# Optimization experiments

Measured on AMD Instinct MI355X. Metric: run time of the kernel, lower is better.

The kernel has to match this reference:

```python
import jax, jax.numpy as jnp
import numpy as np

K = 8  # knn_graph(k=8, loop=True): self-loop kept, so self is among the k nearest


def knn_idx(x, k):
    # x: [N, F]. Pairwise squared distances via the expansion trick.
    x2 = jnp.sum(x * x, axis=-1)                      # [N]
    d = x2[:, None] + x2[None, :] - 2.0 * (x @ x.T)   # [N, N]
    _, idx = jax.lax.top_k(-d, k)                     # [N, k] nearest (incl. self)
    return idx


def edge_conv(x, idx, W1, b1, W2, b2):
    # PyG EdgeConv: message = nn(cat([x_i, x_j - x_i])), aggr='max'.
    # Every node has exactly k incoming edges, so scatter-max == max over the k axis.
    n, f = x.shape
    k = idx.shape[1]
    xi = x[:, None, :]                                # [N, 1, F] center
    xj = x[idx]                                       # [N, k, F] neighbors (gather)
    e = jnp.concatenate([jnp.broadcast_to(xi, (n, k, f)), xj - xi], axis=-1)  # [N,k,2F]
    h = jax.nn.relu(e @ W1 + b1) @ W2 + b2            # [N, k, out]
    return jnp.max(h, axis=1)                         # [N, out]


def setup_inputs() -> dict:
    key = jax.random.key(0)
    ks = jax.random.split(key, 9)
    B, N, F = 2, 4096, 3
    H0, H1, OUT = 64, 128, 256

    def lin(kw, fan_in, fan_out):
        bound = 1.0 / np.sqrt(fan_in)
        kw1, kw2 = jax.random.split(kw)
        W = jax.random.uniform(kw1, (fan_in, fan_out), jnp.float32, -bound, bound)
        b = jax.random.uniform(kw2, (fan_out,), jnp.float32, -bound, bound)
        return W, b

    W1, b1 = lin(ks[0], 2 * F, H0)
    W2, b2 = lin(ks[1], H0, H1)
    W3, b3 = lin(ks[2], 2 * H1, H1)
    W4, b4 = lin(ks[3], H1, OUT)
    point_cloud = jax.random.normal(ks[4], (B, N, F), jnp.float32)
    return {"point_cloud": point_cloud, "W1": W1, "b1": b1, "W2": W2, "b2": b2,
            "W3": W3, "b3": b3, "W4": W4, "b4": b4}


def reference(point_cloud, W1, b1, W2, b2, W3, b3, W4, b4):
    B, N, F = point_cloud.shape
    pts = point_cloud.reshape(B * N, F)               # knn over ALL B*N points (no batch vec)
    idx = knn_idx(jax.lax.stop_gradient(pts), K)      # [B*N, K]
    x = jax.nn.relu(edge_conv(pts, idx, W1, b1, W2, b2))
    x = edge_conv(x, idx, W3, b3, W4, b4)
    return x.reshape(B, N, -1)
```

## Files before the change

### kernel.cpp

```cpp
#include <hip/hip_runtime.h>

#define NPTS 8192
#define NSLICE 64
#define SLICE_LEN (NPTS / NSLICE)
#define KNN 8
#define SURV_CAP 32
#define TQ 32

typedef short bf16x8 __attribute__((ext_vector_type(8)));
typedef float f32x4 __attribute__((ext_vector_type(4)));

__device__ __forceinline__ unsigned short f2bf(float x) {
  unsigned int u = __float_as_uint(x);
  return (unsigned short)((u + 0x7FFF + ((u >> 16) & 1)) >> 16);
}
__device__ __forceinline__ float bf2f(unsigned short s) {
  return __uint_as_float(((unsigned int)s) << 16);
}

__device__ __forceinline__ float dist_exact(float qx, float qy, float qz,
                                            float q2, float px, float py,
                                            float pz, float p2) {
#pragma clang fp contract(off)
  float dot = __fmaf_rn(qz, pz, __fmaf_rn(qy, py, __fmul_rn(qx, px)));
  float t1 = __fadd_rn(q2, p2);
  return __fadd_rn(t1, __fmul_rn(-2.0f, dot));
}

__device__ __forceinline__ float norm2_exact(float x, float y, float z) {
#pragma clang fp contract(off)
  return __fadd_rn(__fadd_rn(__fmul_rn(x, x), __fmul_rn(y, y)),
                   __fmul_rn(z, z));
}

__device__ __forceinline__ float med3(float a, float b, float c) {
  return __builtin_amdgcn_fmed3f(a, b, c);
}

__device__ __forceinline__ double pack_key(float d, int idx) {
  unsigned int ub = __float_as_uint(d);
  ub ^= (((unsigned int)((int)ub >> 31)) | 0x80000000u);
  unsigned int lo = (ub << 13) | (unsigned int)idx;
  unsigned int hi = 0x3ff00000u | (ub >> 19);
  return __hiloint2double((int)hi, (int)lo);
}

#define KEY_DECL                                                            \
  const double KINF = __longlong_as_double(0x7ff0000000000000LL);           \
  double k0 = KINF, k1 = KINF, k2 = KINF, k3 = KINF, k4 = KINF, k5 = KINF,  \
         k6 = KINF, k7 = KINF;
#define KB1(s)                                                              \
  {                                                                         \
    double mn = fmin(carry, k##s);                                          \
    carry = fmax(carry, k##s);                                              \
    k##s = mn;                                                              \
  }
#define KEY_INSERT(key)                                                     \
  {                                                                         \
    double carry = (key);                                                   \
    KB1(0) KB1(1) KB1(2) KB1(3) KB1(4) KB1(5) KB1(6) KB1(7)                 \
  }

#define VINS(dv)                                                            \
  {                                                                         \
    float dd = (dv);                                                        \
    v7 = med3(dd, v6, v7);                                                  \
    v6 = med3(dd, v5, v6);                                                  \
    v5 = med3(dd, v4, v5);                                                  \
    v4 = med3(dd, v3, v4);                                                  \
    v3 = med3(dd, v2, v3);                                                  \
    v2 = med3(dd, v1, v2);                                                  \
    v1 = med3(dd, v0, v1);                                                  \
    v0 = fminf(dd, v0);                                                     \
  }

#define VDECL                                                               \
  const float FINF = __uint_as_float(0x7f800000u);                          \
  float v0 = FINF, v1 = FINF, v2 = FINF, v3 = FINF, v4 = FINF, v5 = FINF,   \
        v6 = FINF, v7 = FINF;

__global__ __launch_bounds__(256) void prep_kernel(
    const float* __restrict__ W4, const float* __restrict__ pts,
    unsigned short* __restrict__ W4ht, unsigned short* __restrict__ W4lt,
    float4* __restrict__ pts4) {
  const int id = blockIdx.x * 256 + threadIdx.x;
  const int k = id >> 8, c = id & 255;
  float v = W4[k * 256 + c];
  unsigned short hi = f2bf(v);
  unsigned short lo = f2bf(v - bf2f(hi));
  W4ht[c * 128 + k] = hi;
  W4lt[c * 128 + k] = lo;
  if (id < NPTS) {
    float x = pts[id * 3 + 0];
    float y = pts[id * 3 + 1];
    float z = pts[id * 3 + 2];
    pts4[id] = make_float4(x, y, z, norm2_exact(x, y, z));
  }
}

__global__ __launch_bounds__(256) void knn_vals_kernel(
    const float4* __restrict__ pts4, float* __restrict__ part_v) {
  __shared__ float4 sp[SLICE_LEN];
  const int t = threadIdx.x;
  const int q = blockIdx.x * 256 + t;
  const int jbase = blockIdx.y * SLICE_LEN;
  for (int p = t; p < SLICE_LEN; p += 256) sp[p] = pts4[jbase + p];
  __syncthreads();
  const float4 qp = pts4[q];
  const float qx = qp.x, qy = qp.y, qz = qp.z, q2 = qp.w;
  VDECL;
  for (int p = 0; p < SLICE_LEN; p += 8) {
    float4 c0 = sp[p + 0];
    float4 c1 = sp[p + 1];
    float4 c2 = sp[p + 2];
    float4 c3 = sp[p + 3];
    float4 c4 = sp[p + 4];
    float4 c5 = sp[p + 5];
    float4 c6 = sp[p + 6];
    float4 c7 = sp[p + 7];
    float d0 = dist_exact(qx, qy, qz, q2, c0.x, c0.y, c0.z, c0.w);
    float d1 = dist_exact(qx, qy, qz, q2, c1.x, c1.y, c1.z, c1.w);
    float d2 = dist_exact(qx, qy, qz, q2, c2.x, c2.y, c2.z, c2.w);
    float d3 = dist_exact(qx, qy, qz, q2, c3.x, c3.y, c3.z, c3.w);
    float d4 = dist_exact(qx, qy, qz, q2, c4.x, c4.y, c4.z, c4.w);
    float d5 = dist_exact(qx, qy, qz, q2, c5.x, c5.y, c5.z, c5.w);
    float d6 = dist_exact(qx, qy, qz, q2, c6.x, c6.y, c6.z, c6.w);
    float d7 = dist_exact(qx, qy, qz, q2, c7.x, c7.y, c7.z, c7.w);
    VINS(d0);
    VINS(d1);
    VINS(d2);
    VINS(d3);
    VINS(d4);
    VINS(d5);
    VINS(d6);
    VINS(d7);
  }
  float* o = &part_v[(size_t)(blockIdx.y * 8) * NPTS + q];
  o[0 * NPTS] = v0;
  o[1 * NPTS] = v1;
  o[2 * NPTS] = v2;
  o[3 * NPTS] = v3;
  o[4 * NPTS] = v4;
  o[5 * NPTS] = v5;
  o[6 * NPTS] = v6;
  o[7 * NPTS] = v7;
}

__global__ __launch_bounds__(256) void knn_thresh_kernel(
    const float* __restrict__ part_v, float* __restrict__ thr,
    unsigned long long* __restrict__ mask) {
  __shared__ float v8s[TQ][8][9];
  __shared__ float smin[TQ][65];
  const int t = threadIdx.x;
  const int lq = t >> 3, c = t & 7;
  const int q = blockIdx.x * TQ + lq;
  {
    VDECL;
#pragma unroll
    for (int s8 = 0; s8 < 8; ++s8) {
      const int s = c * 8 + s8;
      const float* col = &part_v[(size_t)(s * 8) * NPTS + q];
      float a0 = col[0 * (size_t)NPTS];
      float a1 = col[1 * (size_t)NPTS];
      float a2 = col[2 * (size_t)NPTS];
      float a3 = col[3 * (size_t)NPTS];
      float a4 = col[4 * (size_t)NPTS];
      float a5 = col[5 * (size_t)NPTS];
      float a6 = col[6 * (size_t)NPTS];
      float a7 = col[7 * (size_t)NPTS];
      smin[lq][s] = a0;
      VINS(a0);
      VINS(a1);
      VINS(a2);
      VINS(a3);
      VINS(a4);
      VINS(a5);
      VINS(a6);
      VINS(a7);
    }
    v8s[lq][c][0] = v0;
    v8s[lq][c][1] = v1;
    v8s[lq][c][2] = v2;
    v8s[lq][c][3] = v3;
    v8s[lq][c][4] = v4;
    v8s[lq][c][5] = v5;
    v8s[lq][c][6] = v6;
    v8s[lq][c][7] = v7;
  }
  __syncthreads();
  if (c == 0) {
    VDECL;
#pragma unroll
    for (int s = 0; s < 8; ++s) {
      VINS(v8s[lq][s][0]);
      VINS(v8s[lq][s][1]);
      VINS(v8s[lq][s][2]);
      VINS(v8s[lq][s][3]);
      VINS(v8s[lq][s][4]);
      VINS(v8s[lq][s][5]);
      VINS(v8s[lq][s][6]);
      VINS(v8s[lq][s][7]);
    }
    const float tcol = v7 + fabsf(v7) * 4e-5f + 1e-20f;
    const float tmask = v7 + fabsf(v7) * 8e-5f + 2e-20f;
    unsigned long long mk = 0;
#pragma unroll
    for (int s = 0; s < NSLICE; ++s) {
      if (smin[lq][s] <= tmask) mk |= (1ull << s);
    }
    thr[q] = tcol;
    mask[q] = mk;
  }
}

__global__ __launch_bounds__(256) void knn_collect_kernel(
    const float4* __restrict__ pts4, const float* __restrict__ thr,
    const unsigned long long* __restrict__ mask, int* __restrict__ nbr) {
  __shared__ double keybuf[4][SURV_CAP];
  __shared__ int scnt[4];
  const int t = threadIdx.x;
  const int wv = t >> 6;
  const int lane = t & 63;
  const int q = blockIdx.x * 4 + wv;
  if (lane == 0) scnt[wv] = 0;
  __syncthreads();
  const float4 qp = pts4[q];
  const float qx = qp.x, qy = qp.y, qz = qp.z, q2 = qp.w;
  const float thrq = thr[q];
  unsigned long long m = mask[q];
  while (m) {
    const int s = (int)__ffsll(m) - 1;
    m &= m - 1;
    const int base = s * SLICE_LEN;
#pragma unroll
    for (int r = 0; r < SLICE_LEN / 64; ++r) {
      const int j = base + r * 64 + lane;
      const float4 cp = pts4[j];
      const float d = dist_exact(qx, qy, qz, q2, cp.x, cp.y, cp.z, cp.w);
      if (d <= thrq) {
        int slot = atomicAdd(&scnt[wv], 1);
        if (slot < SURV_CAP) keybuf[wv][slot] = pack_key(d, j);
      }
    }
  }
  __syncthreads();
  if (lane == 0) {
    int c = scnt[wv];
    if (c > SURV_CAP) c = SURV_CAP;
    KEY_DECL;
    for (int u = 0; u < c; ++u) {
      KEY_INSERT(keybuf[wv][u]);
    }
    int* o = &nbr[q * KNN];
    o[0] = __double2loint(k0) & 0x1fff;
    o[1] = __double2loint(k1) & 0x1fff;
    o[2] = __double2loint(k2) & 0x1fff;
    o[3] = __double2loint(k3) & 0x1fff;
    o[4] = __double2loint(k4) & 0x1fff;
    o[5] = __double2loint(k5) & 0x1fff;
    o[6] = __double2loint(k6) & 0x1fff;
    o[7] = __double2loint(k7) & 0x1fff;
  }
}

__global__ __launch_bounds__(256) void gemm1_fused_kernel(
    const float* __restrict__ pts, const int* __restrict__ nbr,
    const float* __restrict__ W1, const float* __restrict__ b1,
    const float* __restrict__ W2, const float* __restrict__ b2,
    float* __restrict__ y) {
  __shared__ float es[64][6];
  __shared__ float W1s[6][64];
  __shared__ float b1s[64];
  __shared__ float As[64][64];
  __shared__ float Bs[64][64];
  const int t = threadIdx.x;
  const int rowBase = blockIdx.y * 64;
  const int colBase = blockIdx.x * 64;

  for (int idx = t; idx < 384; idx += 256) W1s[idx >> 6][idx & 63] = W1[idx];
  if (t < 64) b1s[t] = b1[t];
  {
    int cq = t & 15, kr = t >> 4;
#pragma unroll
    for (int it = 0; it < 4; ++it) {
      int k = it * 16 + kr;
      *(float4*)&Bs[k][cq * 4] =
          *(const float4*)&W2[(size_t)k * 128 + colBase + cq * 4];
    }
  }
  if (t < 64) {
    int e = rowBase + t;
    int i = e >> 3;
    int j = nbr[e];
    float xi0 = pts[i * 3], xi1 = pts[i * 3 + 1], xi2 = pts[i * 3 + 2];
    es[t][0] = xi0;
    es[t][1] = xi1;
    es[t][2] = xi2;
    es[t][3] = pts[j * 3] - xi0;
    es[t][4] = pts[j * 3 + 1] - xi1;
    es[t][5] = pts[j * 3 + 2] - xi2;
  }
  __syncthreads();

  {
    const int e = t & 63, k0 = (t >> 6) * 16;
    const float f0 = es[e][0], f1 = es[e][1], f2 = es[e][2];
    const float f3 = es[e][3], f4 = es[e][4], f5 = es[e][5];
#pragma unroll
    for (int k = 0; k < 16; ++k) {
      int c = k0 + k;
      float v = b1s[c];
      v = fmaf(f0, W1s[0][c], v);
      v = fmaf(f1, W1s[1][c], v);
      v = fmaf(f2, W1s[2][c], v);
      v = fmaf(f3, W1s[3][c], v);
      v = fmaf(f4, W1s[4][c], v);
      v = fmaf(f5, W1s[5][c], v);
      As[c][e] = fmaxf(v, 0.0f);
    }
  }
  __syncthreads();

  const int tx = t & 15, ty = t >> 4;
  float acc[4][4] = {};
#pragma unroll 8
  for (int k = 0; k < 64; ++k) {
    float4 a = *(const float4*)&As[k][ty * 4];
    float4 b = *(const float4*)&Bs[k][tx * 4];
    const float ar[4] = {a.x, a.y, a.z, a.w};
    const float br[4] = {b.x, b.y, b.z, b.w};
#pragma unroll
    for (int i = 0; i < 4; ++i)
#pragma unroll
      for (int jj = 0; jj < 4; ++jj)
        acc[i][jj] = fmaf(ar[i], br[jj], acc[i][jj]);
  }
  __syncthreads();

  float* Mx = &As[0][0];
#pragma unroll
  for (int jj = 0; jj < 4; ++jj) {
    float m =
        fmaxf(fmaxf(acc[0][jj], acc[1][jj]), fmaxf(acc[2][jj], acc[3][jj]));
    Mx[ty * 64 + tx * 4 + jj] = m;
  }
  __syncthreads();
  if (t < 128) {
    int p = t >> 4, cq = t & 15;
    int c = cq * 4;
    float4 o;
    float* oa = (float*)&o;
#pragma unroll
    for (int jj = 0; jj < 4; ++jj) {
      float v = fmaxf(Mx[(2 * p) * 64 + c + jj], Mx[(2 * p + 1) * 64 + c + jj]);
      v += b2[colBase + c + jj];
      oa[jj] = fmaxf(v, 0.0f);
    }
    *(float4*)&y[(size_t)(blockIdx.y * 8 + p) * 128 + colBase + c] = o;
  }
}

__global__ __launch_bounds__(256) void gemm_ac_kernel(
    const float* __restrict__ A, const float* __restrict__ W3,
    const float* __restrict__ bias, float* __restrict__ out) {
  __shared__ float As[64][64];
  __shared__ float Bs[64][64];
  const int t = threadIdx.x;
  const int tx = t & 15, ty = t >> 4;
  const int rowBase = blockIdx.y * 64;
  const int colBase = blockIdx.x * 64;
  const float4* A4 = (const float4*)A;
  float acc[4][4] = {};
  const int K = 128, Nglob = 256;

  for (int k0 = 0; k0 < K; k0 += 64) {
#pragma unroll
    for (int it = 0; it < 4; ++it) {
      int idx = it * 256 + t;
      int row = idx & 63, kq = idx >> 6;
      float4 av = A4[(size_t)(rowBase + row) * (K >> 2) + (k0 >> 2) + kq];
      As[kq * 4 + 0][row] = av.x;
      As[kq * 4 + 1][row] = av.y;
      As[kq * 4 + 2][row] = av.z;
      As[kq * 4 + 3][row] = av.w;
    }
#pragma unroll
    for (int it = 0; it < 4; ++it) {
      int idx = it * 256 + t;
      int cq = idx & 15, kr = idx >> 4;
      const float* src =
          (colBase < 128)
              ? &W3[(size_t)(k0 + kr) * 128 + colBase]
              : &W3[(size_t)(128 + k0 + kr) * 128 + (colBase - 128)];
      float4 bv = *(const float4*)&src[cq * 4];
      *(float4*)&Bs[kr][cq * 4] = bv;
    }
    __syncthreads();
#pragma unroll 8
    for (int k = 0; k < 64; ++k) {
      float4 a = *(const float4*)&As[k][ty * 4];
      float4 b = *(const float4*)&Bs[k][tx * 4];
      const float ar[4] = {a.x, a.y, a.z, a.w};
      const float br[4] = {b.x, b.y, b.z, b.w};
#pragma unroll
      for (int i = 0; i < 4; ++i)
#pragma unroll
        for (int jj = 0; jj < 4; ++jj)
          acc[i][jj] = fmaf(ar[i], br[jj], acc[i][jj]);
    }
    __syncthreads();
  }

#pragma unroll
  for (int i = 0; i < 4; ++i) {
    float4 o;
    float* oa = (float*)&o;
#pragma unroll
    for (int jj = 0; jj < 4; ++jj) {
      float v = acc[i][jj];
      int cg = colBase + tx * 4 + jj;
      if (cg < 128) v += bias[cg];
      oa[jj] = v;
    }
    *(float4*)&out[(size_t)(rowBase + ty * 4 + i) * Nglob + colBase + tx * 4] =
        o;
  }
}

__global__ __launch_bounds__(256) void gemm2_mfma_kernel(
    const float* __restrict__ AC, const int* __restrict__ nbr,
    const unsigned short* __restrict__ W4ht,
    const unsigned short* __restrict__ W4lt, const float* __restrict__ b4,
    float* __restrict__ out) {
  __shared__ unsigned short H2h[128 * 40];
  __shared__ unsigned short H2l[128 * 40];
  __shared__ unsigned short Wth[128 * 40];
  __shared__ unsigned short Wtl[128 * 40];
  const int t = threadIdx.x;
  const int rowBase = blockIdx.y * 128;
  const int colBase = blockIdx.x * 128;
  const int eloc = t >> 1, hh = t & 1;
  const int kb = hh * 16;
  const int edge = rowBase + eloc;
  const int ip = edge >> 3;
  const int jp = nbr[edge];
  const float* ai_p = AC + (size_t)ip * 256;
  const float* ci_p = ai_p + 128;
  const float* cj_p = AC + (size_t)jp * 256 + 128;
  const int lane = t & 63;
  const int w = t >> 6;
  const int q = lane >> 4;
  const int nidx = lane & 15;

  f32x4 acc[2][8];
#pragma unroll
  for (int mt = 0; mt < 2; ++mt)
#pragma unroll
    for (int nt = 0; nt < 8; ++nt) acc[mt][nt] = (f32x4){0.f, 0.f, 0.f, 0.f};

  for (int p = 0; p < 4; ++p) {
    const int k0 = p * 32;
    {
      float h2[16];
      const float4* a4 = (const float4*)(ai_p + k0 + kb);
      const float4* c4 = (const float4*)(ci_p + k0 + kb);
      const float4* d4 = (const float4*)(cj_p + k0 + kb);
#pragma unroll
      for (int u = 0; u < 4; ++u) {
        float4 a = a4[u], c = c4[u], d = d4[u];
        h2[u * 4 + 0] = fmaxf(a.x + d.x - c.x, 0.f);
        h2[u * 4 + 1] = fmaxf(a.y + d.y - c.y, 0.f);
        h2[u * 4 + 2] = fmaxf(a.z + d.z - c.z, 0.f);
        h2[u * 4 + 3] = fmaxf(a.w + d.w - c.w, 0.f);
      }
      unsigned int hp[8], lp[8];
#pragma unroll
      for (int u = 0; u < 8; ++u) {
        unsigned short h0 = f2bf(h2[2 * u]), h1 = f2bf(h2[2 * u + 1]);
        hp[u] = (unsigned int)h0 | ((unsigned int)h1 << 16);
        unsigned short l0 = f2bf(h2[2 * u] - bf2f(h0));
        unsigned short l1 = f2bf(h2[2 * u + 1] - bf2f(h1));
        lp[u] = (unsigned int)l0 | ((unsigned int)l1 << 16);
      }
      *(uint4*)&H2h[eloc * 40 + kb] = make_uint4(hp[0], hp[1], hp[2], hp[3]);
      *(uint4*)&H2h[eloc * 40 + kb + 8] =
          make_uint4(hp[4], hp[5], hp[6], hp[7]);
      *(uint4*)&H2l[eloc * 40 + kb] = make_uint4(lp[0], lp[1], lp[2], lp[3]);
      *(uint4*)&H2l[eloc * 40 + kb + 8] =
          make_uint4(lp[4], lp[5], lp[6], lp[7]);
    }
    {
      const size_t src = (size_t)(colBase + eloc) * 128 + k0 + kb;
      *(uint4*)&Wth[eloc * 40 + kb] = *(const uint4*)&W4ht[src];
      *(uint4*)&Wth[eloc * 40 + kb + 8] = *(const uint4*)&W4ht[src + 8];
      *(uint4*)&Wtl[eloc * 40 + kb] = *(const uint4*)&W4lt[src];
      *(uint4*)&Wtl[eloc * 40 + kb + 8] = *(const uint4*)&W4lt[src + 8];
    }
    __syncthreads();
    bf16x8 ah[2], al[2];
#pragma unroll
    for (int mt = 0; mt < 2; ++mt) {
      int row = w * 32 + mt * 16 + nidx;
      ah[mt] = *(const bf16x8*)&H2h[row * 40 + q * 8];
      al[mt] = *(const bf16x8*)&H2l[row * 40 + q * 8];
    }
#pragma unroll
    for (int nt = 0; nt < 8; ++nt) {
      int col = nt * 16 + nidx;
      bf16x8 bh = *(const bf16x8*)&Wth[col * 40 + q * 8];
      bf16x8 bl = *(const bf16x8*)&Wtl[col * 40 + q * 8];
#pragma unroll
      for (int mt = 0; mt < 2; ++mt) {
        acc[mt][nt] = __builtin_amdgcn_mfma_f32_16x16x32_bf16(
            ah[mt], bh, acc[mt][nt], 0, 0, 0);
        acc[mt][nt] = __builtin_amdgcn_mfma_f32_16x16x32_bf16(
            ah[mt], bl, acc[mt][nt], 0, 0, 0);
        acc[mt][nt] = __builtin_amdgcn_mfma_f32_16x16x32_bf16(
            al[mt], bh, acc[mt][nt], 0, 0, 0);
      }
    }
    __syncthreads();
  }

#pragma unroll
  for (int mt = 0; mt < 2; ++mt) {
    const int ebase = rowBase + w * 32 + mt * 16;
    const int pt0 = ebase >> 3;
#pragma unroll
    for (int nt = 0; nt < 8; ++nt) {
      f32x4 a = acc[mt][nt];
      float m = fmaxf(fmaxf(a[0], a[1]), fmaxf(a[2], a[3]));
      float o = fmaxf(m, __shfl_xor(m, 16, 64));
      int cg = colBase + nt * 16 + nidx;
      if (q == 0) {
        out[(size_t)pt0 * 256 + cg] = o + b4[cg];
      } else if (q == 2) {
        out[(size_t)(pt0 + 1) * 256 + cg] = o + b4[cg];
      }
    }
  }
}

extern "C" void kernel_launch(void* const* d_in, const int* in_sizes, int n_in,
                              void* d_out, int out_size, void* d_ws,
                              size_t ws_size, hipStream_t stream) {
  const float* pts = (const float*)d_in[0];
  const float* W1 = (const float*)d_in[1];
  const float* b1 = (const float*)d_in[2];
  const float* W2 = (const float*)d_in[3];
  const float* b2 = (const float*)d_in[4];
  const float* W3 = (const float*)d_in[5];
  const float* b3 = (const float*)d_in[6];
  const float* W4 = (const float*)d_in[7];
  const float* b4 = (const float*)d_in[8];
  float* out = (float*)d_out;

  float* w = (float*)d_ws;
  float* part_v = w;
  float* thr = w + 4194304;
  int* nbr = (int*)(w + 4202496);
  float* y = w + 4268032;
  unsigned long long* mask = (unsigned long long*)(w + 5316608);
  unsigned short* W4ht = (unsigned short*)(w + 5332992);
  unsigned short* W4lt = (unsigned short*)(w + 5349376);
  float4* pts4 = (float4*)(w + 5365760);
  float* AC = w;

  prep_kernel<<<128, 256, 0, stream>>>(W4, pts, W4ht, W4lt, pts4);

  knn_vals_kernel<<<dim3(32, NSLICE), 256, 0, stream>>>(pts4, part_v);
  knn_thresh_kernel<<<NPTS / TQ, 256, 0, stream>>>(part_v, thr, mask);
  knn_collect_kernel<<<2048, 256, 0, stream>>>(pts4, thr, mask, nbr);

  gemm1_fused_kernel<<<dim3(2, 1024), 256, 0, stream>>>(pts, nbr, W1, b1, W2,
                                                        b2, y);

  gemm_ac_kernel<<<dim3(4, 128), 256, 0, stream>>>(y, W3, b3, AC);
  gemm2_mfma_kernel<<<dim3(2, 512), 256, 0, stream>>>(AC, nbr, W4ht, W4lt, b4,
                                                      out);
}
```

Measured before the change: 175.6 us.

## Keep only top-2 per KNN slice and loosen threshold, raising survivor cap

The per-slice distance kernel now keeps only the two smallest distances per query instead of eight, so each candidate costs one med3 and one min instead of an eight-step insertion chain. It also writes a quarter of the partial output. The threshold kernel takes the 8th smallest of these 128 per-slice values, which is still a valid upper bound on the true 8th-nearest distance but a looser one. More candidates can pass, so the survivor capacity grows from 32 to 48, at the cost of more work and possible overflow handling later. An unused alternative VINS macro is defined and immediately undefined.

```diff
diff --git a/kernel.cpp b/kernel.cpp
--- a/kernel.cpp
+++ b/kernel.cpp
@@ -4,7 +4,7 @@
 #define NSLICE 64
 #define SLICE_LEN (NPTS / NSLICE)
 #define KNN 8
-#define SURV_CAP 32
+#define SURV_CAP 48
 #define TQ 32
 
 typedef short bf16x8 __attribute__((ext_vector_type(8)));
@@ -61,6 +61,20 @@
     KB1(0) KB1(1) KB1(2) KB1(3) KB1(4) KB1(5) KB1(6) KB1(7)                 \
   }
 
+#define VINS(dv)                                                            \
+  {                                                                         \
+    float dd = (dv);                                                        \
+    v7 = med3(dd, v6, v7);                                                  \
+    v6 = med3(dd, v5, v6);                                                  \
+    v5 = med3(dd, v4, v5);                                                  \
+    v4 = med3(dd, v3, v4);                                                  \
+    v3 = med3(dd, v2, v2 < dd ? dd : v3);                                   \
+    v2 = med3(dd, v1, v2);                                                  \
+    v1 = med3(dd, v0, v1);                                                  \
+    v0 = fminf(dd, v0);                                                     \
+  }
+
+#undef VINS
 #define VINS(dv)                                                            \
   {                                                                         \
     float dd = (dv);                                                        \
@@ -78,6 +92,13 @@
   const float FINF = __uint_as_float(0x7f800000u);                          \
   float v0 = FINF, v1 = FINF, v2 = FINF, v3 = FINF, v4 = FINF, v5 = FINF,   \
         v6 = FINF, v7 = FINF;
+
+#define VINS2(dv)                                                           \
+  {                                                                         \
+    float dd = (dv);                                                        \
+    s1 = med3(dd, s0, s1);                                                  \
+    s0 = fminf(dd, s0);                                                     \
+  }
 
 __global__ __launch_bounds__(256) void prep_kernel(
     const float* __restrict__ W4, const float* __restrict__ pts,
@@ -108,7 +129,8 @@
   __syncthreads();
   const float4 qp = pts4[q];
   const float qx = qp.x, qy = qp.y, qz = qp.z, q2 = qp.w;
-  VDECL;
+  const float FINF = __uint_as_float(0x7f800000u);
+  float s0 = FINF, s1 = FINF;
   for (int p = 0; p < SLICE_LEN; p += 8) {
     float4 c0 = sp[p + 0];
     float4 c1 = sp[p + 1];
@@ -126,24 +148,18 @@
     float d5 = dist_exact(qx, qy, qz, q2, c5.x, c5.y, c5.z, c5.w);
     float d6 = dist_exact(qx, qy, qz, q2, c6.x, c6.y, c6.z, c6.w);
     float d7 = dist_exact(qx, qy, qz, q2, c7.x, c7.y, c7.z, c7.w);
-    VINS(d0);
-    VINS(d1);
-    VINS(d2);
-    VINS(d3);
-    VINS(d4);
-    VINS(d5);
-    VINS(d6);
-    VINS(d7);
-  }
-  float* o = &part_v[(size_t)(blockIdx.y * 8) * NPTS + q];
-  o[0 * NPTS] = v0;
-  o[1 * NPTS] = v1;
-  o[2 * NPTS] = v2;
-  o[3 * NPTS] = v3;
-  o[4 * NPTS] = v4;
-  o[5 * NPTS] = v5;
-  o[6 * NPTS] = v6;
-  o[7 * NPTS] = v7;
+    VINS2(d0);
+    VINS2(d1);
+    VINS2(d2);
+    VINS2(d3);
+    VINS2(d4);
+    VINS2(d5);
+    VINS2(d6);
+    VINS2(d7);
+  }
+  float* o = &part_v[(size_t)(blockIdx.y * 2) * NPTS + q];
+  o[0 * NPTS] = s0;
+  o[1 * NPTS] = s1;
 }
 
 __global__ __launch_bounds__(256) void knn_thresh_kernel(
@@ -159,24 +175,12 @@
 #pragma unroll
     for (int s8 = 0; s8 < 8; ++s8) {
       const int s = c * 8 + s8;
-      const float* col = &part_v[(size_t)(s * 8) * NPTS + q];
+      const float* col = &part_v[(size_t)(s * 2) * NPTS + q];
       float a0 = col[0 * (size_t)NPTS];
       float a1 = col[1 * (size_t)NPTS];
-      float a2 = col[2 * (size_t)NPTS];
-      float a3 = col[3 * (size_t)NPTS];
-      float a4 = col[4 * (size_t)NPTS];
-      float a5 = col[5 * (size_t)NPTS];
-      float a6 = col[6 * (size_t)NPTS];
-      float a7 = col[7 * (size_t)NPTS];
       smin[lq][s] = a0;
       VINS(a0);
       VINS(a1);
-      VINS(a2);
-      VINS(a3);
-      VINS(a4);
-      VINS(a5);
-      VINS(a6);
-      VINS(a7);
     }
     v8s[lq][c][0] = v0;
     v8s[lq][c][1] = v1;
```

Measured after the change: 161.7 us. 1.09x faster.
